# Performance work log

Measured on AMD Instinct MI355X. Metric: run time of the kernel, lower is better.

The kernel has to match this reference:

```python
import jax, jax.numpy as jnp
import numpy as np

N = 16384

def setup_inputs() -> dict:
    key = jax.random.key(0)
    k1, k2 = jax.random.split(key)
    inputs = jax.random.normal(k1, (N,), dtype=jnp.float32)
    targets = jax.random.randint(k2, (N,), 0, 2)  # int, values in {0,1}
    return {"inputs": inputs, "targets": targets}

def reference(inputs, targets):
    # Flatten, split logits into positives (targets==1) and negatives (targets==0).
    x = inputs.reshape(-1)
    t = targets.reshape(-1).astype(jnp.float32)
    pos_mask = (t == 1.0).astype(x.dtype)  # (N,)
    neg_mask = (t == 0.0).astype(x.dtype)  # (N,)
    # BCE-with-logits against target=1 on diff = x_i - x_j is softplus(-diff).
    # Masked full NxN formulation (jit-friendly, same math as pos/neg outer diff).
    diff = x[:, None] - x[None, :]                      # (N, N)
    pair_w = pos_mask[:, None] * neg_mask[None, :]      # 1 for (pos, neg) pairs
    loss_sum = jnp.sum(jax.nn.softplus(-diff) * pair_w)
    n_pairs = jnp.sum(pair_w)
    # Original returns 0.0 if no pos or no neg examples.
    return jnp.where(n_pairs > 0, loss_sum / jnp.maximum(n_pairs, 1.0), 0.0)
```

## Files before the change

### kernel.cpp

```cpp
#include <hip/hip_runtime.h>


#define PT    512
#define RB    32
#define NWAVE (PT / 64)

template<int NQ>
__device__ __forceinline__ float row_stream(const float* __restrict__ lds_emp,
                                            const float4* __restrict__ x4,
                                            const int4* __restrict__ t4,
                                            int n4, int tid) {
    float emp[NQ * 8];
#pragma unroll
    for (int r = 0; r < NQ * 8; ++r) emp[r] = lds_emp[r];
    float acc[NQ];
#pragma unroll
    for (int q = 0; q < NQ; ++q) acc[q] = 0.f;

    auto do_col = [&](float xc, int tc) {
        const float en = (tc == 0) ? __expf(xc) : 0.f;
#pragma unroll
        for (int q = 0; q < NQ; ++q) {
            float p0 = __builtin_fmaf(en, emp[q * 8 + 0], 1.f);
            p0 *= __builtin_fmaf(en, emp[q * 8 + 1], 1.f);
            p0 *= __builtin_fmaf(en, emp[q * 8 + 2], 1.f);
            p0 *= __builtin_fmaf(en, emp[q * 8 + 3], 1.f);
            float p1 = __builtin_fmaf(en, emp[q * 8 + 4], 1.f);
            p1 *= __builtin_fmaf(en, emp[q * 8 + 5], 1.f);
            p1 *= __builtin_fmaf(en, emp[q * 8 + 6], 1.f);
            p1 *= __builtin_fmaf(en, emp[q * 8 + 7], 1.f);
            acc[q] += __log2f(p0 * p1);
        }
    };

#pragma unroll 2
    for (int v = tid; v < n4; v += PT) {
        const float4 xv = x4[v];
        const int4   tv = t4[v];
        do_col(xv.x, tv.x);
        do_col(xv.y, tv.y);
        do_col(xv.z, tv.z);
        do_col(xv.w, tv.w);
    }
    float s = 0.f;
#pragma unroll
    for (int q = 0; q < NQ; ++q) s += acc[q];
    return s;
}

__global__ __launch_bounds__(PT)
void pair_masked(const float* __restrict__ x, const int* __restrict__ tg,
                 int n, double* __restrict__ wpart) {
    __shared__ float lds_emp[RB];
    __shared__ int lds_k;
    const int bid = blockIdx.x, tid = threadIdx.x;
    const int lane = tid & 63, wid = tid >> 6;
    const int rbase = bid * RB;

    if (wid == 0) {
        float ex = 0.f; int isp = 0;
        if (lane < RB) {
            const int t = tg[rbase + lane];
            isp = (t == 1);
            if (isp) ex = __expf(-x[rbase + lane]);
        }
        const unsigned long long m = __ballot(isp);
        if (lane < RB) lds_emp[lane] = 0.f;
        const int rank = (int)__popcll(m & ((1ull << lane) - 1ull));
        if (isp) lds_emp[rank] = ex;
        if (lane == 0) lds_k = (int)__popcll(m);
    }
    __syncthreads();

    const int kq = (lds_k + 7) >> 3;
    const int gw = bid * NWAVE + wid;
    if (kq == 0) {
        if (lane == 0) wpart[gw] = 0.0;
        return;
    }

    const float4* x4 = (const float4*)x;
    const int4*   t4 = (const int4*)tg;
    const int n4 = n >> 2;
    float s;
    switch (kq) {
        case 1:  s = row_stream<1>(lds_emp, x4, t4, n4, tid); break;
        case 2:  s = row_stream<2>(lds_emp, x4, t4, n4, tid); break;
        case 3:  s = row_stream<3>(lds_emp, x4, t4, n4, tid); break;
        default: s = row_stream<4>(lds_emp, x4, t4, n4, tid); break;
    }

#pragma unroll
    for (int off = 32; off > 0; off >>= 1) s += __shfl_down(s, off, 64);
    if (lane == 0) wpart[gw] = (double)s;
}

__global__ __launch_bounds__(1024)
void finalize_kernel(const int* __restrict__ tg, int n,
                     const double* __restrict__ wpart, int nw,
                     float* __restrict__ out) {
    const int tid = threadIdx.x;
    int cp = 0, cn = 0;
    const int4* t4 = (const int4*)tg;
    for (int v = tid; v < (n >> 2); v += 1024) {
        const int4 t = t4[v];
        cp += (t.x == 1) + (t.y == 1) + (t.z == 1) + (t.w == 1);
        cn += (t.x == 0) + (t.y == 0) + (t.z == 0) + (t.w == 0);
    }
    double d = 0.0;
    for (int k = tid; k < nw; k += 1024) d += wpart[k];
    int c = cp | (cn << 16);
#pragma unroll
    for (int off = 32; off > 0; off >>= 1) {
        d += __shfl_down(d, off, 64);
        c += __shfl_down(c, off, 64);
    }
    __shared__ double fs[16];
    __shared__ int    fc[16];
    if ((tid & 63) == 0) { fs[tid >> 6] = d; fc[tid >> 6] = c; }
    __syncthreads();
    if (tid == 0) {
        double ssum = 0.0; int tot = 0;
#pragma unroll
        for (int w = 0; w < 16; ++w) { ssum += fs[w]; tot += fc[w]; }
        const int np = tot & 0xffff, nn = tot >> 16;
        const double npairs = (double)np * (double)nn;
        out[0] = (npairs > 0.0) ? (float)(ssum * 0.6931471805599453 / npairs) : 0.0f;
    }
}

extern "C" void kernel_launch(void* const* d_in, const int* in_sizes, int n_in,
                              void* d_out, int out_size, void* d_ws, size_t ws_size,
                              hipStream_t stream) {
    const float* x  = (const float*)d_in[0];
    const int*   tg = (const int*)d_in[1];
    const int n = in_sizes[0];

    double* wpart = (double*)d_ws;
    const int nblocks = (n + RB - 1) / RB;
    const int nw = nblocks * NWAVE;

    pair_masked<<<nblocks, PT, 0, stream>>>(x, tg, n, wpart);
    finalize_kernel<<<1, 1024, 0, stream>>>(tg, n, wpart, nw, (float*)d_out);
}
```

Baseline: 20.83 us.

## Fuse finalize into pair kernel via last-block atomic counter reduction

Merges the separate finalize kernel into the main pairwise kernel. Each block reduces its waves to one partial in shared memory and signals completion through two levels of atomic counters (32 group counters, then one global counter). The last block to finish counts positives and negatives and writes the final loss. This removes a second kernel launch and the gap between kernels. In exchange it relies on the workspace counters starting at zero and on modulo counting to stay valid across repeated calls. The inner column loop unroll is also raised from 2 to 4.

```diff
diff --git a/kernel.cpp b/kernel.cpp
--- a/kernel.cpp
+++ b/kernel.cpp
@@ -1,9 +1,9 @@
 #include <hip/hip_runtime.h>
 
 
-#define PT    512
-#define RB    32
-#define NWAVE (PT / 64)
+#define PT   512
+#define RB   32
+#define NL1  32
 
 template<int NQ>
 __device__ __forceinline__ float row_stream(const float* __restrict__ lds_emp,
@@ -33,7 +33,7 @@
         }
     };
 
-#pragma unroll 2
+#pragma unroll 4
     for (int v = tid; v < n4; v += PT) {
         const float4 xv = x4[v];
         const int4   tv = t4[v];
@@ -49,12 +49,18 @@
 }
 
 __global__ __launch_bounds__(PT)
-void pair_masked(const float* __restrict__ x, const int* __restrict__ tg,
-                 int n, double* __restrict__ wpart) {
-    __shared__ float lds_emp[RB];
-    __shared__ int lds_k;
+void ranking_bce_one(const float* __restrict__ x, const int* __restrict__ tg, int n,
+                     double* __restrict__ partials, unsigned* __restrict__ c1,
+                     unsigned* __restrict__ c2, float* __restrict__ out) {
+    __shared__ float  lds_emp[RB];
+    __shared__ int    lds_k;
+    __shared__ double wsum[PT / 64];
+    __shared__ double fs[PT / 64];
+    __shared__ int    fc[PT / 64];
+    __shared__ int    lastFlag;
     const int bid = blockIdx.x, tid = threadIdx.x;
     const int lane = tid & 63, wid = tid >> 6;
+    const int nblocks = (int)gridDim.x;
     const int rbase = bid * RB;
 
     if (wid == 0) {
@@ -73,59 +79,70 @@
     __syncthreads();
 
     const int kq = (lds_k + 7) >> 3;
-    const int gw = bid * NWAVE + wid;
-    if (kq == 0) {
-        if (lane == 0) wpart[gw] = 0.0;
-        return;
-    }
-
-    const float4* x4 = (const float4*)x;
-    const int4*   t4 = (const int4*)tg;
-    const int n4 = n >> 2;
-    float s;
-    switch (kq) {
-        case 1:  s = row_stream<1>(lds_emp, x4, t4, n4, tid); break;
-        case 2:  s = row_stream<2>(lds_emp, x4, t4, n4, tid); break;
-        case 3:  s = row_stream<3>(lds_emp, x4, t4, n4, tid); break;
-        default: s = row_stream<4>(lds_emp, x4, t4, n4, tid); break;
+    float s = 0.f;
+    if (kq > 0) {
+        const float4* x4 = (const float4*)x;
+        const int4*   t4 = (const int4*)tg;
+        const int n4 = n >> 2;
+        switch (kq) {
+            case 1:  s = row_stream<1>(lds_emp, x4, t4, n4, tid); break;
+            case 2:  s = row_stream<2>(lds_emp, x4, t4, n4, tid); break;
+            case 3:  s = row_stream<3>(lds_emp, x4, t4, n4, tid); break;
+            default: s = row_stream<4>(lds_emp, x4, t4, n4, tid); break;
+        }
     }
 
 #pragma unroll
     for (int off = 32; off > 0; off >>= 1) s += __shfl_down(s, off, 64);
-    if (lane == 0) wpart[gw] = (double)s;
-}
-
-__global__ __launch_bounds__(1024)
-void finalize_kernel(const int* __restrict__ tg, int n,
-                     const double* __restrict__ wpart, int nw,
-                     float* __restrict__ out) {
-    const int tid = threadIdx.x;
-    int cp = 0, cn = 0;
-    const int4* t4 = (const int4*)tg;
-    for (int v = tid; v < (n >> 2); v += 1024) {
-        const int4 t = t4[v];
-        cp += (t.x == 1) + (t.y == 1) + (t.z == 1) + (t.w == 1);
-        cn += (t.x == 0) + (t.y == 0) + (t.z == 0) + (t.w == 0);
-    }
-    double d = 0.0;
-    for (int k = tid; k < nw; k += 1024) d += wpart[k];
-    int c = cp | (cn << 16);
-#pragma unroll
-    for (int off = 32; off > 0; off >>= 1) {
-        d += __shfl_down(d, off, 64);
-        c += __shfl_down(c, off, 64);
-    }
-    __shared__ double fs[16];
-    __shared__ int    fc[16];
-    if ((tid & 63) == 0) { fs[tid >> 6] = d; fc[tid >> 6] = c; }
+    if (lane == 0) wsum[wid] = (double)s;
     __syncthreads();
     if (tid == 0) {
-        double ssum = 0.0; int tot = 0;
+        double b = 0.0;
 #pragma unroll
-        for (int w = 0; w < 16; ++w) { ssum += fs[w]; tot += fc[w]; }
-        const int np = tot & 0xffff, nn = tot >> 16;
-        const double npairs = (double)np * (double)nn;
-        out[0] = (npairs > 0.0) ? (float)(ssum * 0.6931471805599453 / npairs) : 0.0f;
+        for (int w = 0; w < PT / 64; ++w) b += wsum[w];
+        partials[bid] = b;
+        __threadfence();
+        int lf = 0;
+        const int g = bid & (NL1 - 1);
+        const unsigned t1 = (unsigned)((nblocks - g + NL1 - 1) / NL1);
+        const unsigned o1 = __hip_atomic_fetch_add(&c1[g], 1u, __ATOMIC_ACQ_REL,
+                                                   __HIP_MEMORY_SCOPE_AGENT);
+        if ((o1 + 1u) % t1 == 0u) {
+            const unsigned o2 = __hip_atomic_fetch_add(c2, 1u, __ATOMIC_ACQ_REL,
+                                                       __HIP_MEMORY_SCOPE_AGENT);
+            if ((o2 + 1u) % (unsigned)NL1 == 0u) lf = 1;
+        }
+        lastFlag = lf;
+    }
+    __syncthreads();
+
+    if (lastFlag) {
+        __threadfence();
+        int cp = 0, cn = 0;
+        const int4* t4 = (const int4*)tg;
+        for (int v = tid; v < (n >> 2); v += PT) {
+            const int4 t = t4[v];
+            cp += (t.x == 1) + (t.y == 1) + (t.z == 1) + (t.w == 1);
+            cn += (t.x == 0) + (t.y == 0) + (t.z == 0) + (t.w == 0);
+        }
+        double d = 0.0;
+        for (int k = tid; k < nblocks; k += PT) d += partials[k];
+        int c = cp | (cn << 16);
+#pragma unroll
+        for (int off = 32; off > 0; off >>= 1) {
+            d += __shfl_down(d, off, 64);
+            c += __shfl_down(c, off, 64);
+        }
+        if (lane == 0) { fs[wid] = d; fc[wid] = c; }
+        __syncthreads();
+        if (tid == 0) {
+            double ssum = 0.0; int tot = 0;
+#pragma unroll
+            for (int w = 0; w < PT / 64; ++w) { ssum += fs[w]; tot += fc[w]; }
+            const int np = tot & 0xffff, nn = tot >> 16;
+            const double npairs = (double)np * (double)nn;
+            out[0] = (npairs > 0.0) ? (float)(ssum * 0.6931471805599453 / npairs) : 0.0f;
+        }
     }
 }
 
@@ -136,10 +153,12 @@
     const int*   tg = (const int*)d_in[1];
     const int n = in_sizes[0];
 
-    double* wpart = (double*)d_ws;
+    char* ws = (char*)d_ws;
+    double*   partials = (double*)(ws);
+    unsigned* c1       = (unsigned*)(ws + 8192);
+    unsigned* c2       = (unsigned*)(ws + 8192 + 128);
+
     const int nblocks = (n + RB - 1) / RB;
-    const int nw = nblocks * NWAVE;
-
-    pair_masked<<<nblocks, PT, 0, stream>>>(x, tg, n, wpart);
-    finalize_kernel<<<1, 1024, 0, stream>>>(tg, n, wpart, nw, (float*)d_out);
+    ranking_bce_one<<<nblocks, PT, 0, stream>>>(x, tg, n, partials, c1, c2,
+                                                (float*)d_out);
 }
```

After: 32.16 us. 54.4% more time.
